# Optimization experiments

Hardware: AMD Instinct MI355X
Metric: run time of the kernel (lower is better)

Reference implementation:

```python
import jax, jax.numpy as jnp
import numpy as np

E = 32      # num_embodiments
A = 64      # action_dim
H = 1024    # hidden_size
B = 64
T = 64


def setup_inputs() -> dict:
    key = jax.random.key(0)
    ks = jax.random.split(key, 9)
    return {
        "actions": jax.random.normal(ks[0], (B, T, A), dtype=jnp.float32),
        "W1_W": 0.02 * jax.random.normal(ks[1], (E, A, H), dtype=jnp.float32),
        "W1_b": jnp.zeros((E, H), dtype=jnp.float32),
        "W2_W": 0.02 * jax.random.normal(ks[2], (E, 2 * H, H), dtype=jnp.float32),
        "W2_b": jnp.zeros((E, H), dtype=jnp.float32),
        "W3_W": 0.02 * jax.random.normal(ks[3], (E, H, H), dtype=jnp.float32),
        "W3_b": jnp.zeros((E, H), dtype=jnp.float32),
        "timesteps": jax.random.randint(ks[4], (B,), 0, 1000, dtype=jnp.int32),
        "cat_ids": jax.random.randint(ks[5], (B,), 0, E, dtype=jnp.int32),
    }


def _cat_linear(x, W, b, cat_ids):
    # x: (B,T,in), W: (E,in,out), b: (E,out)
    Wg = W[cat_ids]               # (B,in,out) gathered per-batch weights
    bg = b[cat_ids]               # (B,out)
    return jnp.einsum('bti,bio->bto', x, Wg) + bg[:, None, :]


def _sinusoidal_pe(t, dim):
    # t: (B,T) float -> (B,T,dim)
    half = dim // 2
    exponent = -jnp.arange(half, dtype=jnp.float32) * (jnp.log(jnp.float32(10000.0)) / half)
    freqs = t[..., None] * jnp.exp(exponent)
    return jnp.concatenate([jnp.sin(freqs), jnp.cos(freqs)], axis=-1)


def reference(actions, W1_W, W1_b, W2_W, W2_b, W3_W, W3_b, timesteps, cat_ids):
    b, t, _ = actions.shape
    ts = jnp.broadcast_to(timesteps.astype(jnp.float32)[:, None], (b, t))  # (B,T)
    a_emb = _cat_linear(actions, W1_W, W1_b, cat_ids)                      # (B,T,H)
    tau_emb = _sinusoidal_pe(ts, H).astype(a_emb.dtype)                    # (B,T,H)
    x = jnp.concatenate([a_emb, tau_emb], axis=-1)                         # (B,T,2H)
    h = _cat_linear(x, W2_W, W2_b, cat_ids)
    x = h * jax.nn.sigmoid(h)                                              # swish
    return _cat_linear(x, W3_W, W3_b, cat_ids)                             # (B,T,H)
```

## Files before the change

kernel.cpp:

```cpp
#include <hip/hip_runtime.h>
#include <hip/hip_bf16.h>

#define NB 64
#define NT 64
#define NA 64
#define NH 1024
#define NE 32
#define K2DIM 2048

typedef unsigned short bf16_t;
typedef __attribute__((ext_vector_type(8))) short bf16x8;
typedef __attribute__((ext_vector_type(4))) short s16x4;
typedef __attribute__((ext_vector_type(4))) float f32x4;

__device__ __forceinline__ bf16_t f32_to_bf16(float f) {
    unsigned int u = __float_as_uint(f);
    u = (u + 0x7FFFu + ((u >> 16) & 1u)) >> 16;
    return (bf16_t)u;
}
__device__ __forceinline__ unsigned cvt2(float x, float y) {
    unsigned short a = __builtin_bit_cast(unsigned short, __float2bfloat16(x));
    unsigned short b = __builtin_bit_cast(unsigned short, __float2bfloat16(y));
    return (unsigned)a | ((unsigned)b << 16);
}

__global__ __launch_bounds__(256) void k1_embed(
    const float* __restrict__ actions, const float* __restrict__ W1,
    const float* __restrict__ b1, const int* __restrict__ timesteps,
    const int* __restrict__ cat_ids, bf16_t* __restrict__ x)
{
    __shared__ float act[NT][NA];
    __shared__ float pe[64];

    const int b   = blockIdx.x;
    const int c0  = blockIdx.y * 64;
    const int tid = threadIdx.x;
    const int cat = cat_ids[b];
    const float ts = (float)timesteps[b];

    const float* ab = actions + b * (NT * NA);
    #pragma unroll
    for (int p = 0; p < 16; ++p) {
        int idx = tid + p * 256;
        act[idx >> 6][idx & 63] = ab[idx];
    }
    if (tid < 64) {
        const float kfreq = logf(10000.0f) / 512.0f;
        int c = c0 + tid;
        float v;
        if (c < 512) v = sinf(ts * expf(-(float)c * kfreq));
        else         v = cosf(ts * expf(-(float)(c - 512) * kfreq));
        pe[tid] = v;
    }
    __syncthreads();

    const int cc = tid & 63;
    const int c  = c0 + cc;
    const int t0 = tid >> 6;

    float acc[16];
    const float bias = b1[cat * NH + c];
    #pragma unroll
    for (int i = 0; i < 16; ++i) acc[i] = bias;

    const float* Wp = W1 + (size_t)cat * (NA * NH) + c;
    #pragma unroll 8
    for (int k = 0; k < NA; ++k) {
        float w = Wp[(size_t)k * NH];
        #pragma unroll
        for (int i = 0; i < 16; ++i)
            acc[i] = fmaf(act[t0 + 4 * i][k], w, acc[i]);
    }

    bf16_t* xb = x + (size_t)b * (NT * K2DIM);
    const bf16_t pv = f32_to_bf16(pe[cc]);
    #pragma unroll
    for (int i = 0; i < 16; ++i) {
        int t = t0 + 4 * i;
        xb[(size_t)t * K2DIM + c]      = f32_to_bf16(acc[i]);
        xb[(size_t)t * K2DIM + NH + c] = pv;
    }
}

template<int KDIM, bool SWISH, typename OutT>
__global__ __launch_bounds__(256, 2) void gemm_mfma(
    const bf16_t* __restrict__ xin, const float* __restrict__ W,
    const float* __restrict__ bias, const int* __restrict__ cat_ids,
    OutT* __restrict__ out)
{
    __shared__ __align__(128) char xs[64 * 128];
    __shared__ __align__(128) char wsm[16384];

    const int b    = blockIdx.x;
    const int n0   = blockIdx.y * 128;
    const int tid  = threadIdx.x;
    const int lane = tid & 63;
    const int wv   = tid >> 6;
    const int cat  = cat_ids[b];

    const int mw = (wv & 1) * 32;
    const int nw = (wv >> 1) * 64;
    const int pw = (wv >> 1) * 4;
    const int l15 = lane & 15;
    const int l4  = lane >> 4;

    const bf16_t* xb = xin + (size_t)b * (size_t)NT * KDIM;
    const float*  Wb = W + (size_t)cat * KDIM * NH + n0;

    f32x4 acc[2][4];
    #pragma unroll
    for (int nf = 0; nf < 4; ++nf) {
        float bv = bias[(size_t)cat * NH + n0 + nw + nf * 16 + l15];
        acc[0][nf] = (f32x4){bv, bv, bv, bv};
        acc[1][nf] = acc[0][nf];
    }

    const unsigned wbase = (unsigned)(unsigned long long)&wsm[0];
    const unsigned laneB = wbase + (unsigned)(l4 * 2048 + l15 * 8);

    for (int kc = 0; kc < KDIM / 64; ++kc) {
        const bf16_t* xsrc = xb + kc * 64;
        const float*  Wp   = Wb + (size_t)(kc * 64) * NH;

        __syncthreads();

        #pragma unroll
        for (int p = 0; p < 2; ++p) {
            int id = tid + p * 256;
            int t  = id >> 3;
            int k8 = id & 7;
            uint4 v = *(const uint4*)(xsrc + (size_t)t * KDIM + k8 * 8);
            int off = (t * 128 + k8 * 16) ^ ((t & 7) << 4);
            *(uint4*)(xs + off) = v;
        }
        #pragma unroll
        for (int p = 0; p < 4; ++p) {
            int id  = tid + p * 256;
            int k   = id >> 4;
            int oct = id & 15;
            const float* src = Wp + (size_t)k * NH + oct * 8;
            float4 w0 = *(const float4*)(src);
            float4 w1 = *(const float4*)(src + 4);
            uint4 pk;
            pk.x = cvt2(w0.x, w0.y);
            pk.y = cvt2(w0.z, w0.w);
            pk.z = cvt2(w1.x, w1.y);
            pk.w = cvt2(w1.z, w1.w);
            int off = ((k >> 2) * 8 + (oct >> 1)) * 128 + (k & 3) * 32 + (oct & 1) * 16;
            *(uint4*)(wsm + off) = pk;
        }
        __syncthreads();

        #pragma unroll
        for (int ks = 0; ks < 2; ++ks) {
            bf16x8 af[2];
            #pragma unroll
            for (int m = 0; m < 2; ++m) {
                int row = mw + m * 16 + l15;
                int off = (row * 128 + ks * 64 + l4 * 16) ^ ((row & 7) << 4);
                af[m] = *(const bf16x8*)(xs + off);
            }
            bf16x8 bfr[4];
            #pragma unroll
            for (int nf = 0; nf < 4; ++nf) {
                unsigned a = laneB + (unsigned)(ks * 8192 + (pw + nf) * 128);
                s16x4 lo, hi;
                asm volatile("ds_read_b64_tr_b16 %0, %1" : "=v"(lo) : "v"(a));
                asm volatile("ds_read_b64_tr_b16 %0, %1 offset:1024" : "=v"(hi) : "v"(a));
                bfr[nf] = __builtin_shufflevector(lo, hi, 0, 1, 2, 3, 4, 5, 6, 7);
            }
            asm volatile("s_waitcnt lgkmcnt(0)" ::: "memory");
            __builtin_amdgcn_sched_barrier(0);
            #pragma unroll
            for (int m = 0; m < 2; ++m)
                #pragma unroll
                for (int nf = 0; nf < 4; ++nf)
                    acc[m][nf] = __builtin_amdgcn_mfma_f32_16x16x32_bf16(
                        af[m], bfr[nf], acc[m][nf], 0, 0, 0);
        }
    }

    #pragma unroll
    for (int m = 0; m < 2; ++m) {
        #pragma unroll
        for (int nf = 0; nf < 4; ++nf) {
            int col = n0 + nw + nf * 16 + l15;
            #pragma unroll
            for (int r = 0; r < 4; ++r) {
                int row = mw + m * 16 + l4 * 4 + r;
                float h = acc[m][nf][r];
                if (SWISH) h = h / (1.0f + __expf(-h));
                if constexpr (sizeof(OutT) == 2) {
                    out[((size_t)b * NT + row) * NH + col] = (OutT)f32_to_bf16(h);
                } else {
                    out[((size_t)b * NT + row) * NH + col] = h;
                }
            }
        }
    }
}

extern "C" void kernel_launch(void* const* d_in, const int* in_sizes, int n_in,
                              void* d_out, int out_size, void* d_ws, size_t ws_size,
                              hipStream_t stream) {
    const float* actions   = (const float*)d_in[0];
    const float* W1        = (const float*)d_in[1];
    const float* b1        = (const float*)d_in[2];
    const float* W2        = (const float*)d_in[3];
    const float* b2        = (const float*)d_in[4];
    const float* W3        = (const float*)d_in[5];
    const float* b3        = (const float*)d_in[6];
    const int*   timesteps = (const int*)d_in[7];
    const int*   cat_ids   = (const int*)d_in[8];
    float* out = (float*)d_out;

    bf16_t* x = (bf16_t*)d_ws;
    bf16_t* y = x + (size_t)NB * NT * K2DIM;

    k1_embed<<<dim3(NB, NH / 64), 256, 0, stream>>>(actions, W1, b1, timesteps, cat_ids, x);
    gemm_mfma<K2DIM, true,  bf16_t><<<dim3(NB, NH / 128), 256, 0, stream>>>(x, W2, b2, cat_ids, y);
    gemm_mfma<NH,    false, float ><<<dim3(NB, NH / 128), 256, 0, stream>>>(y, W3, b3, cat_ids, out);
}
```

Before: 157.5 us.

## Group batches by embodiment so GEMM blocks share weight tiles

A new single-block kernel sorts batch rows by category and packs them into groups of up to four that share a category. Each 512-thread GEMM block then loads one weight tile and applies it to all batches in its group, so each fp32 weight tile is read and converted to bf16 fewer times. The main loop also prefetches the next chunk into registers while computing the current one. In exchange there is an extra kernel launch, grid slots for empty groups that exit at once, and possible load imbalance when categories are unevenly populated.

```diff
diff --git a/kernel.cpp b/kernel.cpp
--- a/kernel.cpp
+++ b/kernel.cpp
@@ -22,6 +22,56 @@
     unsigned short a = __builtin_bit_cast(unsigned short, __float2bfloat16(x));
     unsigned short b = __builtin_bit_cast(unsigned short, __float2bfloat16(y));
     return (unsigned)a | ((unsigned)b << 16);
+}
+
+__global__ void make_groups(const int* __restrict__ cat_ids,
+                            int* __restrict__ groups)
+{
+    __shared__ int keys[NB], order[NB], catv[NB];
+    __shared__ int gcat[NB], gnb[NB], gb[NB][4];
+    __shared__ int sng;
+
+    const int tid = threadIdx.x;
+    int c = cat_ids[tid];
+    catv[tid] = c;
+    keys[tid] = c * 64 + tid;
+    __syncthreads();
+
+    int mykey = keys[tid];
+    int rank = 0;
+    for (int j = 0; j < NB; ++j) rank += (keys[j] < mykey) ? 1 : 0;
+    order[rank] = tid;
+    __syncthreads();
+
+    if (tid == 0) {
+        int ng = 0, prev = -1, cnt = 4;
+        for (int i = 0; i < NB; ++i) {
+            int b  = order[i];
+            int cb = catv[b];
+            if (cb != prev || cnt == 4) {
+                gcat[ng] = cb; gnb[ng] = 0; cnt = 0; prev = cb; ++ng;
+            }
+            gb[ng - 1][cnt] = b;
+            ++cnt; gnb[ng - 1] = cnt;
+        }
+        sng = ng;
+    }
+    __syncthreads();
+
+    int ng = sng;
+    int base = tid * 8;
+    if (tid < ng) {
+        int nbv = gnb[tid];
+        groups[base + 0] = gcat[tid];
+        groups[base + 1] = nbv;
+        #pragma unroll
+        for (int s = 0; s < 4; ++s)
+            groups[base + 2 + s] = gb[tid][s < nbv ? s : 0];
+        groups[base + 6] = 0; groups[base + 7] = 0;
+    } else {
+        #pragma unroll
+        for (int s = 0; s < 8; ++s) groups[base + s] = 0;
+    }
 }
 
 __global__ __launch_bounds__(256) void k1_embed(
@@ -83,84 +133,110 @@
 }
 
 template<int KDIM, bool SWISH, typename OutT>
-__global__ __launch_bounds__(256, 2) void gemm_mfma(
+__global__ __launch_bounds__(512) void gemm_grouped(
     const bf16_t* __restrict__ xin, const float* __restrict__ W,
-    const float* __restrict__ bias, const int* __restrict__ cat_ids,
+    const float* __restrict__ bias, const int* __restrict__ groups,
     OutT* __restrict__ out)
 {
-    __shared__ __align__(128) char xs[64 * 128];
+    __shared__ __align__(128) char xs[4 * 8192];
     __shared__ __align__(128) char wsm[16384];
 
-    const int b    = blockIdx.x;
+    const int* grp = groups + blockIdx.x * 8;
+    const int nb = grp[1];
+    if (nb == 0) return;
+    const int cat = grp[0];
+    int bslot[4];
+    #pragma unroll
+    for (int s = 0; s < 4; ++s) bslot[s] = grp[2 + s];
+
     const int n0   = blockIdx.y * 128;
     const int tid  = threadIdx.x;
     const int lane = tid & 63;
     const int wv   = tid >> 6;
-    const int cat  = cat_ids[b];
-
-    const int mw = (wv & 1) * 32;
-    const int nw = (wv >> 1) * 64;
-    const int pw = (wv >> 1) * 4;
-    const int l15 = lane & 15;
-    const int l4  = lane >> 4;
-
-    const bf16_t* xb = xin + (size_t)b * (size_t)NT * KDIM;
-    const float*  Wb = W + (size_t)cat * KDIM * NH + n0;
-
-    f32x4 acc[2][4];
+    const int l15  = lane & 15;
+    const int l4   = lane >> 4;
+    const int msl  = wv & 3;
+    const int pw   = (wv >> 2) * 4;
+    const int ncol0 = n0 + (wv >> 2) * 64;
+
+    constexpr int NK = KDIM / 64;
+
+    const int xt  = tid >> 3;
+    const int xk8 = tid & 7;
+    const int xoff = ((xt * 128 + xk8 * 16) ^ ((xt & 7) << 4));
+    const bf16_t* xsrc[4];
+    #pragma unroll
+    for (int p = 0; p < 4; ++p)
+        xsrc[p] = xin + ((size_t)bslot[p] * NT + xt) * KDIM + xk8 * 8;
+    const int wk  = tid >> 4;
+    const int oct = tid & 15;
+    const float* Wt0 = W + (size_t)cat * KDIM * NH + n0
+                         + (size_t)wk * NH + oct * 8;
+    int woff[2];
+    #pragma unroll
+    for (int p = 0; p < 2; ++p) {
+        int kk = wk + 32 * p;
+        woff[p] = ((kk >> 2) * 8 + (oct >> 1)) * 128 + (kk & 3) * 32 + (oct & 1) * 16;
+    }
+
+    f32x4 acc[4][4];
     #pragma unroll
     for (int nf = 0; nf < 4; ++nf) {
-        float bv = bias[(size_t)cat * NH + n0 + nw + nf * 16 + l15];
-        acc[0][nf] = (f32x4){bv, bv, bv, bv};
-        acc[1][nf] = acc[0][nf];
+        float bv = bias[(size_t)cat * NH + ncol0 + nf * 16 + l15];
+        #pragma unroll
+        for (int mf = 0; mf < 4; ++mf)
+            acc[mf][nf] = (f32x4){bv, bv, bv, bv};
     }
 
     const unsigned wbase = (unsigned)(unsigned long long)&wsm[0];
     const unsigned laneB = wbase + (unsigned)(l4 * 2048 + l15 * 8);
-
-    for (int kc = 0; kc < KDIM / 64; ++kc) {
-        const bf16_t* xsrc = xb + kc * 64;
-        const float*  Wp   = Wb + (size_t)(kc * 64) * NH;
-
+    const int aslot = msl * 8192;
+
+    uint4  xr[4];
+    float4 wr[4];
+
+    auto LOAD = [&](int kc) {
+        #pragma unroll
+        for (int p = 0; p < 4; ++p)
+            xr[p] = *(const uint4*)(xsrc[p] + (size_t)kc * 64);
+        #pragma unroll
+        for (int p = 0; p < 2; ++p) {
+            const float* s = Wt0 + (size_t)(kc * 64 + 32 * p) * NH;
+            wr[2 * p]     = *(const float4*)(s);
+            wr[2 * p + 1] = *(const float4*)(s + 4);
+        }
+    };
+    auto WRITE = [&]() {
+        #pragma unroll
+        for (int p = 0; p < 4; ++p)
+            *(uint4*)(xs + xoff + p * 8192) = xr[p];
+        #pragma unroll
+        for (int p = 0; p < 2; ++p) {
+            uint4 pk;
+            pk.x = cvt2(wr[2 * p].x,     wr[2 * p].y);
+            pk.y = cvt2(wr[2 * p].z,     wr[2 * p].w);
+            pk.z = cvt2(wr[2 * p + 1].x, wr[2 * p + 1].y);
+            pk.w = cvt2(wr[2 * p + 1].z, wr[2 * p + 1].w);
+            *(uint4*)(wsm + woff[p]) = pk;
+        }
+    };
+
+    LOAD(0);
+    for (int kc = 0; kc < NK; ++kc) {
         __syncthreads();
-
-        #pragma unroll
-        for (int p = 0; p < 2; ++p) {
-            int id = tid + p * 256;
-            int t  = id >> 3;
-            int k8 = id & 7;
-            uint4 v = *(const uint4*)(xsrc + (size_t)t * KDIM + k8 * 8);
-            int off = (t * 128 + k8 * 16) ^ ((t & 7) << 4);
-            *(uint4*)(xs + off) = v;
-        }
-        #pragma unroll
-        for (int p = 0; p < 4; ++p) {
-            int id  = tid + p * 256;
-            int k   = id >> 4;
-            int oct = id & 15;
-            const float* src = Wp + (size_t)k * NH + oct * 8;
-            float4 w0 = *(const float4*)(src);
-            float4 w1 = *(const float4*)(src + 4);
-            uint4 pk;
-            pk.x = cvt2(w0.x, w0.y);
-            pk.y = cvt2(w0.z, w0.w);
-            pk.z = cvt2(w1.x, w1.y);
-            pk.w = cvt2(w1.z, w1.w);
-            int off = ((k >> 2) * 8 + (oct >> 1)) * 128 + (k & 3) * 32 + (oct & 1) * 16;
-            *(uint4*)(wsm + off) = pk;
-        }
+        WRITE();
         __syncthreads();
+        if (kc + 1 < NK) LOAD(kc + 1);
 
         #pragma unroll
         for (int ks = 0; ks < 2; ++ks) {
-            bf16x8 af[2];
+            bf16x8 af[4], bfr[4];
             #pragma unroll
-            for (int m = 0; m < 2; ++m) {
-                int row = mw + m * 16 + l15;
-                int off = (row * 128 + ks * 64 + l4 * 16) ^ ((row & 7) << 4);
-                af[m] = *(const bf16x8*)(xs + off);
+            for (int mf = 0; mf < 4; ++mf) {
+                int row = mf * 16 + l15;
+                int off = aslot + ((row * 128 + ks * 64 + l4 * 16) ^ ((row & 7) << 4));
+                af[mf] = *(const bf16x8*)(xs + off);
             }
-            bf16x8 bfr[4];
             #pragma unroll
             for (int nf = 0; nf < 4; ++nf) {
                 unsigned a = laneB + (unsigned)(ks * 8192 + (pw + nf) * 128);
@@ -172,28 +248,29 @@
             asm volatile("s_waitcnt lgkmcnt(0)" ::: "memory");
             __builtin_amdgcn_sched_barrier(0);
             #pragma unroll
-            for (int m = 0; m < 2; ++m)
+            for (int mf = 0; mf < 4; ++mf)
                 #pragma unroll
                 for (int nf = 0; nf < 4; ++nf)
-                    acc[m][nf] = __builtin_amdgcn_mfma_f32_16x16x32_bf16(
-                        af[m], bfr[nf], acc[m][nf], 0, 0, 0);
-        }
-    }
-
-    #pragma unroll
-    for (int m = 0; m < 2; ++m) {
+                    acc[mf][nf] = __builtin_amdgcn_mfma_f32_16x16x32_bf16(
+                        af[mf], bfr[nf], acc[mf][nf], 0, 0, 0);
+        }
+    }
+
+    const int bout = bslot[msl];
+    #pragma unroll
+    for (int mf = 0; mf < 4; ++mf) {
         #pragma unroll
         for (int nf = 0; nf < 4; ++nf) {
-            int col = n0 + nw + nf * 16 + l15;
+            int col = ncol0 + nf * 16 + l15;
             #pragma unroll
             for (int r = 0; r < 4; ++r) {
-                int row = mw + m * 16 + l4 * 4 + r;
-                float h = acc[m][nf][r];
+                int trow = mf * 16 + l4 * 4 + r;
+                float h = acc[mf][nf][r];
                 if (SWISH) h = h / (1.0f + __expf(-h));
                 if constexpr (sizeof(OutT) == 2) {
-                    out[((size_t)b * NT + row) * NH + col] = (OutT)f32_to_bf16(h);
+                    out[((size_t)bout * NT + trow) * NH + col] = (OutT)f32_to_bf16(h);
                 } else {
-                    out[((size_t)b * NT + row) * NH + col] = h;
+                    out[((size_t)bout * NT + trow) * NH + col] = h;
                 }
             }
         }
@@ -216,8 +293,10 @@
 
     bf16_t* x = (bf16_t*)d_ws;
     bf16_t* y = x + (size_t)NB * NT * K2DIM;
-
+    int* groups = (int*)(y + (size_t)NB * NT * NH);
+
+    make_groups<<<1, 64, 0, stream>>>(cat_ids, groups);
     k1_embed<<<dim3(NB, NH / 64), 256, 0, stream>>>(actions, W1, b1, timesteps, cat_ids, x);
-    gemm_mfma<K2DIM, true,  bf16_t><<<dim3(NB, NH / 128), 256, 0, stream>>>(x, W2, b2, cat_ids, y);
-    gemm_mfma<NH,    false, float ><<<dim3(NB, NH / 128), 256, 0, stream>>>(y, W3, b3, cat_ids, out);
-}
+    gemm_grouped<K2DIM, true,  bf16_t><<<dim3(64, NH / 128), 512, 0, stream>>>(x, W2, b2, groups, y);
+    gemm_grouped<NH,    false, float ><<<dim3(64, NH / 128), 512, 0, stream>>>(y, W3, b3, groups, out);
+}
```

New measurement: 193.9 us. 23.2% more time.

## Software-pipeline GEMM with double-buffered LDS and direct global-to-LDS activation loads

Applied to the files above, without the earlier changes.

Replaces the single-buffered GEMM kernel with a 512-thread, double-buffered pipeline. Activation tiles go straight from global memory into LDS via global_load_lds, and weight tiles are prefetched into registers two chunks ahead, so loads overlap the MFMA work. The grid is reordered so that consecutive blocks share a batch row and its weights. The aim is to hide global-memory latency and drop one barrier per iteration, at the cost of more LDS, register pressure and delicate manual waitcnt accounting.

```diff
diff --git a/kernel.cpp b/kernel.cpp
--- a/kernel.cpp
+++ b/kernel.cpp
@@ -13,6 +13,9 @@
 typedef __attribute__((ext_vector_type(4))) short s16x4;
 typedef __attribute__((ext_vector_type(4))) float f32x4;
 
+#define AS1 __attribute__((address_space(1)))
+#define AS3 __attribute__((address_space(3)))
+
 __device__ __forceinline__ bf16_t f32_to_bf16(float f) {
     unsigned int u = __float_as_uint(f);
     u = (u + 0x7FFFu + ((u >> 16) & 1u)) >> 16;
@@ -22,6 +25,9 @@
     unsigned short a = __builtin_bit_cast(unsigned short, __float2bfloat16(x));
     unsigned short b = __builtin_bit_cast(unsigned short, __float2bfloat16(y));
     return (unsigned)a | ((unsigned)b << 16);
+}
+__device__ __forceinline__ void gload_lds16(const void* g, void* l) {
+    __builtin_amdgcn_global_load_lds((const AS1 void*)g, (AS3 void*)l, 16, 0, 0);
 }
 
 __global__ __launch_bounds__(256) void k1_embed(
@@ -83,111 +89,136 @@
 }
 
 template<int KDIM, bool SWISH, typename OutT>
-__global__ __launch_bounds__(256, 2) void gemm_mfma(
+__global__ __launch_bounds__(512, 4) void gemm_pipe(
     const bf16_t* __restrict__ xin, const float* __restrict__ W,
     const float* __restrict__ bias, const int* __restrict__ cat_ids,
     OutT* __restrict__ out)
 {
-    __shared__ __align__(128) char xs[64 * 128];
-    __shared__ __align__(128) char wsm[16384];
-
-    const int b    = blockIdx.x;
-    const int n0   = blockIdx.y * 128;
+    __shared__ __align__(128) char lds[2][24576];
+
+    const int b    = blockIdx.y;
+    const int n0   = blockIdx.x * 128;
     const int tid  = threadIdx.x;
     const int lane = tid & 63;
     const int wv   = tid >> 6;
+    const int l15  = lane & 15;
+    const int l4   = lane >> 4;
+    const int wm   = wv >> 2;
+    const int wn   = wv & 3;
     const int cat  = cat_ids[b];
 
-    const int mw = (wv & 1) * 32;
-    const int nw = (wv >> 1) * 64;
-    const int pw = (wv >> 1) * 4;
-    const int l15 = lane & 15;
-    const int l4  = lane >> 4;
-
-    const bf16_t* xb = xin + (size_t)b * (size_t)NT * KDIM;
-    const float*  Wb = W + (size_t)cat * KDIM * NH + n0;
-
-    f32x4 acc[2][4];
-    #pragma unroll
-    for (int nf = 0; nf < 4; ++nf) {
-        float bv = bias[(size_t)cat * NH + n0 + nw + nf * 16 + l15];
+    constexpr int NCH = KDIM / 64;
+
+    const int xt = tid >> 3;
+    const int xj = tid & 7;
+    const bf16_t* xg = xin + ((size_t)b * NT + xt) * KDIM + ((xj ^ (xt & 7)) * 8);
+
+    const int wk  = tid >> 3;
+    const int wo2 = tid & 7;
+    const float* wg = W + (size_t)cat * KDIM * NH + (size_t)wk * NH + n0 + wo2 * 16;
+    const int wloff = 8192 + ((wk >> 2) * 8 + wo2) * 128 + (wk & 3) * 32;
+
+    f32x4 acc[2][2];
+    #pragma unroll
+    for (int nf = 0; nf < 2; ++nf) {
+        float bv = bias[(size_t)cat * NH + n0 + wn * 32 + nf * 16 + l15];
         acc[0][nf] = (f32x4){bv, bv, bv, bv};
         acc[1][nf] = acc[0][nf];
     }
 
-    const unsigned wbase = (unsigned)(unsigned long long)&wsm[0];
-    const unsigned laneB = wbase + (unsigned)(l4 * 2048 + l15 * 8);
-
-    for (int kc = 0; kc < KDIM / 64; ++kc) {
-        const bf16_t* xsrc = xb + kc * 64;
-        const float*  Wp   = Wb + (size_t)(kc * 64) * NH;
-
-        __syncthreads();
-
-        #pragma unroll
-        for (int p = 0; p < 2; ++p) {
-            int id = tid + p * 256;
-            int t  = id >> 3;
-            int k8 = id & 7;
-            uint4 v = *(const uint4*)(xsrc + (size_t)t * KDIM + k8 * 8);
-            int off = (t * 128 + k8 * 16) ^ ((t & 7) << 4);
-            *(uint4*)(xs + off) = v;
+    const unsigned lbase = (unsigned)(unsigned long long)&lds[0][0];
+    const unsigned trb   = lbase + 8192u
+                         + (unsigned)(l4 * 2048 + l15 * 8 + wn * 2 * 128);
+
+    float4 a0, a1, a2, a3, b0, b1, b2, b3;
+
+#define XL(c) do { int i_ = (c) < NCH ? (c) : NCH - 1;                        \
+        gload_lds16(xg + (size_t)i_ * 64,                                     \
+                    &lds[0][0] + ((c) & 1) * 24576 + wv * 1024); } while (0)
+#define WLD(d0,d1,d2,d3,c) do { int i_ = (c) < NCH ? (c) : NCH - 1;           \
+        const float* s_ = wg + (size_t)i_ * 64 * NH;                          \
+        d0 = *(const float4*)(s_);     d1 = *(const float4*)(s_ + 4);         \
+        d2 = *(const float4*)(s_ + 8); d3 = *(const float4*)(s_ + 12); } while (0)
+#define WST(p_, s0,s1,s2,s3) do {                                             \
+        char* bp_ = &lds[0][0] + (p_) * 24576;                                \
+        uint4 k0_, k1_;                                                       \
+        k0_.x = cvt2(s0.x, s0.y); k0_.y = cvt2(s0.z, s0.w);                   \
+        k0_.z = cvt2(s1.x, s1.y); k0_.w = cvt2(s1.z, s1.w);                   \
+        k1_.x = cvt2(s2.x, s2.y); k1_.y = cvt2(s2.z, s2.w);                   \
+        k1_.z = cvt2(s3.x, s3.y); k1_.w = cvt2(s3.z, s3.w);                   \
+        *(uint4*)(bp_ + wloff)      = k0_;                                    \
+        *(uint4*)(bp_ + wloff + 16) = k1_; } while (0)
+
+    auto COMPUTE = [&](int p) {
+        const char* bp = &lds[0][0] + p * 24576;
+        bf16x8 af[2][2];
+        s16x4  lo[2][2], hi[2][2];
+        #pragma unroll
+        for (int ks = 0; ks < 2; ++ks) {
+            #pragma unroll
+            for (int m = 0; m < 2; ++m) {
+                int row = wm * 32 + m * 16 + l15;
+                af[ks][m] = *(const bf16x8*)(bp + row * 128
+                              + (((ks * 4 + l4) ^ (row & 7)) * 16));
+            }
+            #pragma unroll
+            for (int nf = 0; nf < 2; ++nf) {
+                unsigned a = trb + (unsigned)(p * 24576 + ks * 8192 + nf * 128);
+                asm volatile("ds_read_b64_tr_b16 %0, %1" : "=v"(lo[ks][nf]) : "v"(a));
+                asm volatile("ds_read_b64_tr_b16 %0, %1 offset:1024" : "=v"(hi[ks][nf]) : "v"(a));
+            }
         }
-        #pragma unroll
-        for (int p = 0; p < 4; ++p) {
-            int id  = tid + p * 256;
-            int k   = id >> 4;
-            int oct = id & 15;
-            const float* src = Wp + (size_t)k * NH + oct * 8;
-            float4 w0 = *(const float4*)(src);
-            float4 w1 = *(const float4*)(src + 4);
-            uint4 pk;
-            pk.x = cvt2(w0.x, w0.y);
-            pk.y = cvt2(w0.z, w0.w);
-            pk.z = cvt2(w1.x, w1.y);
-            pk.w = cvt2(w1.z, w1.w);
-            int off = ((k >> 2) * 8 + (oct >> 1)) * 128 + (k & 3) * 32 + (oct & 1) * 16;
-            *(uint4*)(wsm + off) = pk;
-        }
-        __syncthreads();
-
-        #pragma unroll
-        for (int ks = 0; ks < 2; ++ks) {
-            bf16x8 af[2];
-            #pragma unroll
-            for (int m = 0; m < 2; ++m) {
-                int row = mw + m * 16 + l15;
-                int off = (row * 128 + ks * 64 + l4 * 16) ^ ((row & 7) << 4);
-                af[m] = *(const bf16x8*)(xs + off);
-            }
-            bf16x8 bfr[4];
-            #pragma unroll
-            for (int nf = 0; nf < 4; ++nf) {
-                unsigned a = laneB + (unsigned)(ks * 8192 + (pw + nf) * 128);
-                s16x4 lo, hi;
-                asm volatile("ds_read_b64_tr_b16 %0, %1" : "=v"(lo) : "v"(a));
-                asm volatile("ds_read_b64_tr_b16 %0, %1 offset:1024" : "=v"(hi) : "v"(a));
-                bfr[nf] = __builtin_shufflevector(lo, hi, 0, 1, 2, 3, 4, 5, 6, 7);
-            }
-            asm volatile("s_waitcnt lgkmcnt(0)" ::: "memory");
-            __builtin_amdgcn_sched_barrier(0);
+        asm volatile("s_waitcnt lgkmcnt(0)" ::: "memory");
+        __builtin_amdgcn_sched_barrier(0);
+        #pragma unroll
+        for (int ks = 0; ks < 2; ++ks)
             #pragma unroll
             for (int m = 0; m < 2; ++m)
                 #pragma unroll
-                for (int nf = 0; nf < 4; ++nf)
+                for (int nf = 0; nf < 2; ++nf) {
+                    bf16x8 bfr = __builtin_shufflevector(
+                        lo[ks][nf], hi[ks][nf], 0, 1, 2, 3, 4, 5, 6, 7);
                     acc[m][nf] = __builtin_amdgcn_mfma_f32_16x16x32_bf16(
-                        af[m], bfr[nf], acc[m][nf], 0, 0, 0);
-        }
-    }
+                        af[ks][m], bfr, acc[m][nf], 0, 0, 0);
+                }
+    };
+
+    XL(0);
+    __builtin_amdgcn_sched_barrier(0);
+    WLD(a0, a1, a2, a3, 0);
+    WLD(b0, b1, b2, b3, 1);
+    WST(0, a0, a1, a2, a3);
+    WLD(a0, a1, a2, a3, 2);
+    asm volatile("s_waitcnt lgkmcnt(0)" ::: "memory");
+
+    for (int kc = 0; kc < NCH; kc += 2) {
+        __builtin_amdgcn_s_barrier();
+        XL(kc + 1);
+        __builtin_amdgcn_sched_barrier(0);
+        WST(1, b0, b1, b2, b3);
+        WLD(b0, b1, b2, b3, kc + 3);
+        COMPUTE(0);
+        asm volatile("s_waitcnt vmcnt(4)" ::: "memory");
+        __builtin_amdgcn_s_barrier();
+        XL(kc + 2);
+        __builtin_amdgcn_sched_barrier(0);
+        WST(0, a0, a1, a2, a3);
+        WLD(a0, a1, a2, a3, kc + 4);
+        COMPUTE(1);
+        asm volatile("s_waitcnt vmcnt(4)" ::: "memory");
+    }
+#undef XL
+#undef WLD
+#undef WST
 
     #pragma unroll
     for (int m = 0; m < 2; ++m) {
         #pragma unroll
-        for (int nf = 0; nf < 4; ++nf) {
-            int col = n0 + nw + nf * 16 + l15;
+        for (int nf = 0; nf < 2; ++nf) {
+            int col = n0 + wn * 32 + nf * 16 + l15;
             #pragma unroll
             for (int r = 0; r < 4; ++r) {
-                int row = mw + m * 16 + l4 * 4 + r;
+                int row = wm * 32 + m * 16 + l4 * 4 + r;
                 float h = acc[m][nf][r];
                 if (SWISH) h = h / (1.0f + __expf(-h));
                 if constexpr (sizeof(OutT) == 2) {
@@ -218,6 +249,6 @@
     bf16_t* y = x + (size_t)NB * NT * K2DIM;
 
     k1_embed<<<dim3(NB, NH / 64), 256, 0, stream>>>(actions, W1, b1, timesteps, cat_ids, x);
-    gemm_mfma<K2DIM, true,  bf16_t><<<dim3(NB, NH / 128), 256, 0, stream>>>(x, W2, b2, cat_ids, y);
-    gemm_mfma<NH,    false, float ><<<dim3(NB, NH / 128), 256, 0, stream>>>(y, W3, b3, cat_ids, out);
-}
+    gemm_pipe<K2DIM, true,  bf16_t><<<dim3(8, 64), 512, 0, stream>>>(x, W2, b2, cat_ids, y);
+    gemm_pipe<NH,    false, float ><<<dim3(8, 64), 512, 0, stream>>>(y, W3, b3, cat_ids, out);
+}
```

New measurement: 173.0 us. 1.1x slower.
